# Optimization experiments

Hardware: AMD Instinct MI355X
Metric: run time of the kernel (lower is better)

Reference implementation:

```python
import jax, jax.numpy as jnp
import numpy as np

K_UP = 5
UP = 2
KS = 3
C_IN = 256


def pixel_shuffle(x, r):
    N, C, H, W = x.shape
    x = x.reshape(N, C // (r * r), r, r, H, W)
    return x.transpose(0, 1, 4, 2, 5, 3).reshape(N, C // (r * r), H * r, W * r)


def conv2d(x, w, b, pad):
    y = jax.lax.conv_general_dilated(
        x, w, window_strides=(1, 1), padding=[(pad, pad), (pad, pad)],
        dimension_numbers=('NCHW', 'OIHW', 'NCHW'))
    return y + b[None, :, None, None]


def setup_inputs() -> dict:
    key = jax.random.key(0)
    ks = jax.random.split(key, 7)
    C = C_IN
    Cd = C // 2
    Ce = UP * UP * K_UP * K_UP  # 100
    x = jax.random.normal(ks[0], (4, C, 64, 64), dtype=jnp.float32)
    # kaiming-normal-ish inits, biases small uniform (torch default)
    w_down = jax.random.normal(ks[1], (Cd, C, 1, 1), dtype=jnp.float32) * np.sqrt(2.0 / C)
    b_down = jax.random.uniform(ks[2], (Cd,), dtype=jnp.float32, minval=-0.05, maxval=0.05)
    w_enc = jax.random.normal(ks[3], (Ce, Cd, KS, KS), dtype=jnp.float32) * np.sqrt(2.0 / (Cd * KS * KS))
    b_enc = jax.random.uniform(ks[4], (Ce,), dtype=jnp.float32, minval=-0.05, maxval=0.05)
    w_out = jax.random.normal(ks[5], (C, C, 1, 1), dtype=jnp.float32) * np.sqrt(2.0 / C)
    b_out = jax.random.uniform(ks[6], (C,), dtype=jnp.float32, minval=-0.05, maxval=0.05)
    return {"x": x, "w_down": w_down, "b_down": b_down, "w_enc": w_enc,
            "b_enc": b_enc, "w_out": w_out, "b_out": b_out}


def reference(x, w_down, b_down, w_enc, b_enc, w_out, b_out):
    N, C, H, W = x.shape
    k2 = K_UP * K_UP  # 25
    u2 = UP * UP      # 4
    # kernel prediction branch
    kt = conv2d(x, w_down, b_down, 0)
    kt = conv2d(kt, w_enc, b_enc, KS // 2)
    kt = pixel_shuffle(kt, UP)              # (N, 25, H*UP, W*UP)
    kt = jax.nn.softmax(kt, axis=1)
    # unfold(2,UP,UP).unfold(3,UP,UP) -> (N,25,H,W,UP,UP) -> (N,H,W,25,UP*UP)
    kt = kt.reshape(N, k2, H, UP, W, UP).transpose(0, 2, 4, 1, 3, 5)
    kt = kt.reshape(N, H, W, k2, u2)
    # feature patches: pad then gather k_up x k_up window per pixel
    pad = K_UP // 2
    xp = jnp.pad(x, ((0, 0), (0, 0), (pad, pad), (pad, pad)))
    patches = jnp.stack(
        [xp[:, :, i:i + H, j:j + W] for i in range(K_UP) for j in range(K_UP)],
        axis=-1)                            # (N, C, H, W, 25)
    # per-pixel weighted sum: (N,H,W,C,25) @ (N,H,W,25,u2)
    out = jnp.einsum('nchwk,nhwkp->nchwp', patches, kt)  # (N,C,H,W,u2)
    out = out.transpose(0, 1, 4, 2, 3).reshape(N, C * u2, H, W)
    out = pixel_shuffle(out, UP)            # (N, C, H*UP, W*UP)
    return conv2d(out, w_out, b_out, 0)
```

## Files before the change

### kernel.cpp

```cpp
#include <hip/hip_runtime.h>
#include <hip/hip_bf16.h>


#define NB    4
#define NPIX  4096

typedef short s16x8 __attribute__((ext_vector_type(8)));
typedef float f32x4 __attribute__((ext_vector_type(4)));

#define MFMA16(a, b, c) __builtin_amdgcn_mfma_f32_16x16x32_bf16((a), (b), (c), 0, 0, 0)

__device__ __forceinline__ ushort f2b(float f) {
    __hip_bfloat16 h = __float2bfloat16(f);
    return *(ushort*)&h;
}
__device__ __forceinline__ float b2f(ushort u) {
    unsigned v = ((unsigned)u) << 16;
    return *(float*)&v;
}

__global__ __launch_bounds__(256) void prep_kernel(
    const float* __restrict__ wd, const float* __restrict__ wo,
    const float* __restrict__ we,
    ushort* __restrict__ wdb, ushort* __restrict__ wob, ushort* __restrict__ wrb)
{
    int idx = blockIdx.x * 256 + threadIdx.x;
    if (idx < 32768) {
        wdb[idx] = f2b(wd[idx]);
    } else if (idx < 98304) {
        int i = idx - 32768;
        wob[i] = f2b(wo[i]);
    } else if (idx < 227328) {
        int i = idx - 98304;
        int co = i / 1152, k = i - co * 1152;
        int tap = k >> 7, c = k & 127;
        float v = (co < 100) ? we[(co * 128 + c) * 9 + tap] : 0.0f;
        wrb[i] = f2b(v);
    }
}

__global__ __launch_bounds__(256) void transpose_cast_kernel(
    const float* __restrict__ X, ushort* __restrict__ Xt)
{
    __shared__ ushort xs[64][264];
    const int n = blockIdx.y, p0 = blockIdx.x * 64;
    const int tid = threadIdx.x;
    const float* Xn = X + (size_t)n * 256 * NPIX;

    #pragma unroll
    for (int j = 0; j < 16; j++) {
        float4 v = *(const float4*)&Xn[(size_t)tid * NPIX + p0 + j * 4];
        xs[j * 4 + 0][tid] = f2b(v.x);
        xs[j * 4 + 1][tid] = f2b(v.y);
        xs[j * 4 + 2][tid] = f2b(v.z);
        xs[j * 4 + 3][tid] = f2b(v.w);
    }
    __syncthreads();
    #pragma unroll
    for (int i = 0; i < 8; i++) {
        int flat = tid + 256 * i;
        int pix = flat >> 5, c16 = flat & 31;
        s16x8 v = *(const s16x8*)&xs[pix][c16 * 8];
        *(s16x8*)&Xt[((size_t)(n * NPIX + p0 + pix)) * 256 + c16 * 8] = v;
    }
}

template<int COUT, bool BIAS>
__global__ __launch_bounds__(256, 1) void gemm_mfma_kernel(
    const ushort* __restrict__ Xt,
    const ushort* __restrict__ Wb,
    const float* __restrict__ bias,
    ushort* __restrict__ Out)
{
    __shared__ ushort xs[64][264];
    const int n = blockIdx.y, p0 = blockIdx.x * 64;
    const int tid = threadIdx.x, lane = tid & 63, wid = tid >> 6;
    const int wp = wid >> 1, wc = wid & 1;
    const int l15 = lane & 15, l4 = lane >> 4;
    const ushort* Xn = Xt + (size_t)(n * NPIX + p0) * 256;

    #pragma unroll
    for (int i = 0; i < 8; i++) {
        int flat = tid + 256 * i;
        int row = flat >> 5, ch = flat & 31;
        s16x8 v = *(const s16x8*)&Xn[row * 256 + ch * 8];
        *(s16x8*)&xs[row][ch * 8] = v;
    }
    __syncthreads();

    constexpr int NCF = COUT / 32;
    const int crow = wc * (COUT / 2);

    f32x4 acc[2][NCF] = {};

    #pragma unroll 2
    for (int ks = 0; ks < 8; ks++) {
        int k0 = ks * 32 + l4 * 8;
        s16x8 a0 = *(const s16x8*)&xs[wp * 32 + l15][k0];
        s16x8 a1 = *(const s16x8*)&xs[wp * 32 + 16 + l15][k0];
        #pragma unroll
        for (int cf = 0; cf < NCF; cf++) {
            s16x8 b = *(const s16x8*)&Wb[(size_t)(crow + cf * 16 + l15) * 256 + k0];
            acc[0][cf] = MFMA16(a0, b, acc[0][cf]);
            acc[1][cf] = MFMA16(a1, b, acc[1][cf]);
        }
    }

    #pragma unroll
    for (int pf = 0; pf < 2; pf++) {
        #pragma unroll
        for (int cf = 0; cf < NCF; cf++) {
            int c = crow + cf * 16 + l15;
            float bb = BIAS ? bias[c] : 0.0f;
            #pragma unroll
            for (int r = 0; r < 4; r++) {
                int pix = p0 + wp * 32 + pf * 16 + l4 * 4 + r;
                Out[(size_t)(n * NPIX + pix) * COUT + c] = f2b(acc[pf][cf][r] + bb);
            }
        }
    }
}

__global__ __launch_bounds__(256, 1) void conv_mfma_kernel(
    const ushort* __restrict__ T1t,
    const ushort* __restrict__ Wr,
    const float* __restrict__ Benc,
    float* __restrict__ E)
{
    __shared__ ushort hs[100][136];
    const int n = blockIdx.y, tile = blockIdx.x;
    const int h0 = (tile >> 3) * 8, w0 = (tile & 7) * 8;
    const int tid = threadIdx.x, lane = tid & 63, wid = tid >> 6;
    const int l15 = lane & 15, l4 = lane >> 4;

    for (int u = tid; u < 1600; u += 256) {
        int hp = u >> 4, ch = u & 15;
        int r = hp / 10, s = hp - r * 10;
        int gh = h0 - 1 + r, gw = w0 - 1 + s;
        s16x8 v = {};
        if ((unsigned)gh < 64u && (unsigned)gw < 64u)
            v = *(const s16x8*)&T1t[((size_t)n * NPIX + gh * 64 + gw) * 128 + ch * 8];
        *(s16x8*)&hs[hp][ch * 8] = v;
    }
    __syncthreads();

    const int pl = wid * 16 + l15;
    const int ph = pl >> 3, pw = pl & 7;

    f32x4 acc[7] = {};

    for (int tap = 0; tap < 9; tap++) {
        int dy = tap / 3, dx = tap - dy * 3;
        int hp = (ph + dy) * 10 + (pw + dx);
        const ushort* hrow = &hs[hp][l4 * 8];
        const ushort* wrow = &Wr[(size_t)l15 * 1152 + tap * 128 + l4 * 8];
        #pragma unroll
        for (int cb = 0; cb < 4; cb++) {
            s16x8 b = *(const s16x8*)&hrow[cb * 32];
            #pragma unroll
            for (int mf = 0; mf < 7; mf++) {
                s16x8 a = *(const s16x8*)&wrow[(size_t)mf * 16 * 1152 + cb * 32];
                acc[mf] = MFMA16(a, b, acc[mf]);
            }
        }
    }

    const int gpix = (h0 + ph) * 64 + w0 + pw;
    #pragma unroll
    for (int mf = 0; mf < 7; mf++) {
        #pragma unroll
        for (int r = 0; r < 4; r++) {
            int co = mf * 16 + l4 * 4 + r;
            if (co < 100)
                E[((size_t)n * 100 + co) * NPIX + gpix] = acc[mf][r] + Benc[co];
        }
    }
}

__global__ __launch_bounds__(256) void carafe_kernel(
    const float* __restrict__ E,
    const ushort* __restrict__ XOt,
    const float* __restrict__ Bout,
    float* __restrict__ Z)
{
    __shared__ __attribute__((aligned(16))) float sm[25][64][4];
    __shared__ float xs[64][145];

    const int n = blockIdx.z, oc = blockIdx.y, tile = blockIdx.x;
    const int th0 = (tile >> 3) * 8, tw0 = (tile & 7) * 8;
    const int tid = threadIdx.x;

    {
        int p = tid & 3, pix = tid >> 2;
        int gh = th0 + (pix >> 3), gw = tw0 + (pix & 7);
        const float* En = E + (size_t)n * 100 * NPIX + gh * 64 + gw;
        float v[25];
        float mx = -1e30f;
        #pragma unroll
        for (int k = 0; k < 25; k++) {
            v[k] = En[(size_t)(k * 4 + p) * NPIX];
            mx = fmaxf(mx, v[k]);
        }
        float s = 0.0f;
        #pragma unroll
        for (int k = 0; k < 25; k++) { v[k] = __expf(v[k] - mx); s += v[k]; }
        float inv = 1.0f / s;
        #pragma unroll
        for (int k = 0; k < 25; k++) sm[k][pix][p] = v[k] * inv;
    }

    for (int u = tid; u < 2304; u += 256) {
        int hp = u >> 4, cg = u & 15;
        int r = hp / 12, s = hp - r * 12;
        int gh = th0 - 2 + r, gw = tw0 - 2 + s;
        float v0 = 0.f, v1 = 0.f, v2 = 0.f, v3 = 0.f;
        if ((unsigned)gh < 64u && (unsigned)gw < 64u) {
            const ushort* src = &XOt[((size_t)n * NPIX + gh * 64 + gw) * 256 + oc * 64 + cg * 4];
            ushort4 raw = *(const ushort4*)src;
            v0 = b2f(raw.x); v1 = b2f(raw.y); v2 = b2f(raw.z); v3 = b2f(raw.w);
        }
        xs[cg * 4 + 0][hp] = v0;
        xs[cg * 4 + 1][hp] = v1;
        xs[cg * 4 + 2][hp] = v2;
        xs[cg * 4 + 3][hp] = v3;
    }
    __syncthreads();

    const int pix = tid & 63;
    const int og = tid >> 6;
    const int ph = pix >> 3, pw = pix & 7;

    float acc[16][4] = {};
    for (int k = 0; k < 25; k++) {
        int di = k / 5, dj = k - di * 5;
        float4 wv = *(const float4*)&sm[k][pix][0];
        int base = (ph + di) * 12 + pw + dj;
        #pragma unroll
        for (int i = 0; i < 16; i++) {
            float xv = xs[og * 16 + i][base];
            acc[i][0] += xv * wv.x;
            acc[i][1] += xv * wv.y;
            acc[i][2] += xv * wv.z;
            acc[i][3] += xv * wv.w;
        }
    }

    const int gh = th0 + ph, gw = tw0 + pw;
    #pragma unroll
    for (int i = 0; i < 16; i++) {
        int o = oc * 64 + og * 16 + i;
        float bb = Bout[o];
        float2 r0 = make_float2(acc[i][0] + bb, acc[i][1] + bb);
        float2 r1 = make_float2(acc[i][2] + bb, acc[i][3] + bb);
        size_t base = (((size_t)n * 256 + o) * 128 + 2 * gh) * 128 + 2 * gw;
        *(float2*)&Z[base]       = r0;
        *(float2*)&Z[base + 128] = r1;
    }
}

extern "C" void kernel_launch(void* const* d_in, const int* in_sizes, int n_in,
                              void* d_out, int out_size, void* d_ws, size_t ws_size,
                              hipStream_t stream) {
    const float* x      = (const float*)d_in[0];
    const float* w_down = (const float*)d_in[1];
    const float* b_down = (const float*)d_in[2];
    const float* w_enc  = (const float*)d_in[3];
    const float* b_enc  = (const float*)d_in[4];
    const float* w_out  = (const float*)d_in[5];
    const float* b_out  = (const float*)d_in[6];
    float* z = (float*)d_out;

    ushort* xT  = (ushort*)d_ws;
    ushort* t1T = xT + 4194304;
    ushort* xoT = t1T + 2097152;
    float*  e   = (float*)(xoT + 4194304);
    ushort* wdb = (ushort*)(e + 1638400);
    ushort* wob = wdb + 32768;
    ushort* wrb = wob + 65536;

    prep_kernel<<<888, 256, 0, stream>>>(w_down, w_out, w_enc, wdb, wob, wrb);
    transpose_cast_kernel<<<dim3(64, NB), 256, 0, stream>>>(x, xT);
    gemm_mfma_kernel<128, true><<<dim3(64, NB), 256, 0, stream>>>(xT, wdb, b_down, t1T);
    gemm_mfma_kernel<256, false><<<dim3(64, NB), 256, 0, stream>>>(xT, wob, nullptr, xoT);
    conv_mfma_kernel<<<dim3(64, NB), 256, 0, stream>>>(t1T, wrb, b_enc, e);
    carafe_kernel<<<dim3(64, 4, NB), 256, 0, stream>>>(e, xoT, b_out, z);
}
```

Measured before the change: 175.9 us.

## Fuse transpose with dual GEMM and fuse encoder conv into CARAFE kernel

The transpose/cast kernel and the two 1x1 GEMMs become a single kernel that reads fp32 X directly and computes both the down projection and the output projection against concatenated weights. The 3x3 encoder conv is fused into the CARAFE kernel, which keeps the encoder logits in shared memory instead of a global fp32 buffer and covers all 256 output channels per block. This cuts launches and removes the round trips through global memory for xT and E. In exchange, the CARAFE grid shrinks from 1024 to 256 blocks, each larger and with serialized phases, so less work runs in parallel and the conv stage uses only half the waves.

New measurement: 170.1 us. -3.3%, faster.

```diff
diff --git a/kernel.cpp b/kernel.cpp
--- a/kernel.cpp
+++ b/kernel.cpp
@@ -22,14 +22,12 @@
 __global__ __launch_bounds__(256) void prep_kernel(
     const float* __restrict__ wd, const float* __restrict__ wo,
     const float* __restrict__ we,
-    ushort* __restrict__ wdb, ushort* __restrict__ wob, ushort* __restrict__ wrb)
+    ushort* __restrict__ wcomb, ushort* __restrict__ wrb)
 {
     int idx = blockIdx.x * 256 + threadIdx.x;
-    if (idx < 32768) {
-        wdb[idx] = f2b(wd[idx]);
-    } else if (idx < 98304) {
-        int i = idx - 32768;
-        wob[i] = f2b(wo[i]);
+    if (idx < 98304) {
+        float v = (idx < 32768) ? wd[idx] : wo[idx - 32768];
+        wcomb[idx] = f2b(v);
     } else if (idx < 227328) {
         int i = idx - 98304;
         int co = i / 1152, k = i - co * 1152;
@@ -39,101 +37,95 @@
     }
 }
 
-__global__ __launch_bounds__(256) void transpose_cast_kernel(
-    const float* __restrict__ X, ushort* __restrict__ Xt)
+__global__ __launch_bounds__(512, 1) void dual_gemm_kernel(
+    const float*  __restrict__ X,
+    const ushort* __restrict__ Wcomb,
+    const float*  __restrict__ b_down,
+    ushort* __restrict__ T1t,
+    ushort* __restrict__ XOt)
 {
-    __shared__ ushort xs[64][264];
-    const int n = blockIdx.y, p0 = blockIdx.x * 64;
-    const int tid = threadIdx.x;
-    const float* Xn = X + (size_t)n * 256 * NPIX;
-
-    #pragma unroll
-    for (int j = 0; j < 16; j++) {
-        float4 v = *(const float4*)&Xn[(size_t)tid * NPIX + p0 + j * 4];
-        xs[j * 4 + 0][tid] = f2b(v.x);
-        xs[j * 4 + 1][tid] = f2b(v.y);
-        xs[j * 4 + 2][tid] = f2b(v.z);
-        xs[j * 4 + 3][tid] = f2b(v.w);
-    }
-    __syncthreads();
-    #pragma unroll
-    for (int i = 0; i < 8; i++) {
-        int flat = tid + 256 * i;
-        int pix = flat >> 5, c16 = flat & 31;
-        s16x8 v = *(const s16x8*)&xs[pix][c16 * 8];
-        *(s16x8*)&Xt[((size_t)(n * NPIX + p0 + pix)) * 256 + c16 * 8] = v;
-    }
-}
-
-template<int COUT, bool BIAS>
-__global__ __launch_bounds__(256, 1) void gemm_mfma_kernel(
-    const ushort* __restrict__ Xt,
-    const ushort* __restrict__ Wb,
-    const float* __restrict__ bias,
-    ushort* __restrict__ Out)
-{
-    __shared__ ushort xs[64][264];
+    __shared__ __attribute__((aligned(16))) ushort xs[64][264];
     const int n = blockIdx.y, p0 = blockIdx.x * 64;
     const int tid = threadIdx.x, lane = tid & 63, wid = tid >> 6;
-    const int wp = wid >> 1, wc = wid & 1;
     const int l15 = lane & 15, l4 = lane >> 4;
-    const ushort* Xn = Xt + (size_t)(n * NPIX + p0) * 256;
-
+    const float* Xn = X + (size_t)n * 256 * NPIX + p0;
+
+    {
+        int c = tid >> 1, half = tid & 1;
+        const float* src = Xn + (size_t)c * NPIX + half * 32;
+        #pragma unroll
+        for (int j = 0; j < 8; j++) {
+            float4 v = *(const float4*)&src[j * 4];
+            int pix = half * 32 + j * 4;
+            xs[pix + 0][c] = f2b(v.x);
+            xs[pix + 1][c] = f2b(v.y);
+            xs[pix + 2][c] = f2b(v.z);
+            xs[pix + 3][c] = f2b(v.w);
+        }
+    }
+    __syncthreads();
+
+    const int wp = wid >> 1;
+    const int wc = wid & 1;
+    const int crow = wc * 192;
+
+    f32x4 acc[12] = {};
     #pragma unroll
-    for (int i = 0; i < 8; i++) {
-        int flat = tid + 256 * i;
-        int row = flat >> 5, ch = flat & 31;
-        s16x8 v = *(const s16x8*)&Xn[row * 256 + ch * 8];
-        *(s16x8*)&xs[row][ch * 8] = v;
-    }
-    __syncthreads();
-
-    constexpr int NCF = COUT / 32;
-    const int crow = wc * (COUT / 2);
-
-    f32x4 acc[2][NCF] = {};
-
-    #pragma unroll 2
     for (int ks = 0; ks < 8; ks++) {
         int k0 = ks * 32 + l4 * 8;
-        s16x8 a0 = *(const s16x8*)&xs[wp * 32 + l15][k0];
-        s16x8 a1 = *(const s16x8*)&xs[wp * 32 + 16 + l15][k0];
-        #pragma unroll
-        for (int cf = 0; cf < NCF; cf++) {
-            s16x8 b = *(const s16x8*)&Wb[(size_t)(crow + cf * 16 + l15) * 256 + k0];
-            acc[0][cf] = MFMA16(a0, b, acc[0][cf]);
-            acc[1][cf] = MFMA16(a1, b, acc[1][cf]);
+        s16x8 a = *(const s16x8*)&xs[wp * 16 + l15][k0];
+        #pragma unroll
+        for (int cf = 0; cf < 12; cf++) {
+            s16x8 b = *(const s16x8*)&Wcomb[(size_t)(crow + cf * 16 + l15) * 256 + k0];
+            acc[cf] = MFMA16(a, b, acc[cf]);
         }
     }
 
     #pragma unroll
-    for (int pf = 0; pf < 2; pf++) {
-        #pragma unroll
-        for (int cf = 0; cf < NCF; cf++) {
-            int c = crow + cf * 16 + l15;
-            float bb = BIAS ? bias[c] : 0.0f;
+    for (int cf = 0; cf < 12; cf++) {
+        int cbase = crow + cf * 16;
+        int c = cbase + l15;
+        if (cbase < 128) {
+            float bb = b_down[c];
             #pragma unroll
             for (int r = 0; r < 4; r++) {
-                int pix = p0 + wp * 32 + pf * 16 + l4 * 4 + r;
-                Out[(size_t)(n * NPIX + pix) * COUT + c] = f2b(acc[pf][cf][r] + bb);
-            }
-        }
-    }
-}
-
-__global__ __launch_bounds__(256, 1) void conv_mfma_kernel(
+                int pix = p0 + wp * 16 + l4 * 4 + r;
+                T1t[(size_t)(n * NPIX + pix) * 128 + c] = f2b(acc[cf][r] + bb);
+            }
+        } else {
+            int c2 = c - 128;
+            #pragma unroll
+            for (int r = 0; r < 4; r++) {
+                int pix = p0 + wp * 16 + l4 * 4 + r;
+                XOt[(size_t)(n * NPIX + pix) * 256 + c2] = f2b(acc[cf][r]);
+            }
+        }
+    }
+}
+
+#define SMEM_A 27264
+#define SMEM_TOTAL (SMEM_A + 74240)
+
+__global__ __launch_bounds__(512, 1) void carafe_fused_kernel(
     const ushort* __restrict__ T1t,
     const ushort* __restrict__ Wr,
-    const float* __restrict__ Benc,
-    float* __restrict__ E)
+    const float*  __restrict__ Benc,
+    const ushort* __restrict__ XOt,
+    const float*  __restrict__ Bout,
+    float* __restrict__ Z)
 {
-    __shared__ ushort hs[100][136];
+    __shared__ __attribute__((aligned(16))) char smem[SMEM_TOTAL];
+    ushort (*hs)[136]   = (ushort(*)[136])smem;
+    float  (*sm)[64][4] = (float(*)[64][4])smem;
+    float  (*eld)[101]  = (float(*)[101])(smem + SMEM_A);
+    float  (*xs)[145]   = (float(*)[145])(smem + SMEM_A);
+
     const int n = blockIdx.y, tile = blockIdx.x;
     const int h0 = (tile >> 3) * 8, w0 = (tile & 7) * 8;
     const int tid = threadIdx.x, lane = tid & 63, wid = tid >> 6;
     const int l15 = lane & 15, l4 = lane >> 4;
 
-    for (int u = tid; u < 1600; u += 256) {
+    for (int u = tid; u < 1600; u += 512) {
         int hp = u >> 4, ch = u & 15;
         int r = hp / 10, s = hp - r * 10;
         int gh = h0 - 1 + r, gw = w0 - 1 + s;
@@ -144,117 +136,102 @@
     }
     __syncthreads();
 
-    const int pl = wid * 16 + l15;
-    const int ph = pl >> 3, pw = pl & 7;
-
-    f32x4 acc[7] = {};
-
-    for (int tap = 0; tap < 9; tap++) {
-        int dy = tap / 3, dx = tap - dy * 3;
-        int hp = (ph + dy) * 10 + (pw + dx);
-        const ushort* hrow = &hs[hp][l4 * 8];
-        const ushort* wrow = &Wr[(size_t)l15 * 1152 + tap * 128 + l4 * 8];
-        #pragma unroll
-        for (int cb = 0; cb < 4; cb++) {
-            s16x8 b = *(const s16x8*)&hrow[cb * 32];
-            #pragma unroll
-            for (int mf = 0; mf < 7; mf++) {
-                s16x8 a = *(const s16x8*)&wrow[(size_t)mf * 16 * 1152 + cb * 32];
-                acc[mf] = MFMA16(a, b, acc[mf]);
-            }
-        }
-    }
-
-    const int gpix = (h0 + ph) * 64 + w0 + pw;
-    #pragma unroll
-    for (int mf = 0; mf < 7; mf++) {
-        #pragma unroll
-        for (int r = 0; r < 4; r++) {
-            int co = mf * 16 + l4 * 4 + r;
-            if (co < 100)
-                E[((size_t)n * 100 + co) * NPIX + gpix] = acc[mf][r] + Benc[co];
-        }
-    }
-}
-
-__global__ __launch_bounds__(256) void carafe_kernel(
-    const float* __restrict__ E,
-    const ushort* __restrict__ XOt,
-    const float* __restrict__ Bout,
-    float* __restrict__ Z)
-{
-    __shared__ __attribute__((aligned(16))) float sm[25][64][4];
-    __shared__ float xs[64][145];
-
-    const int n = blockIdx.z, oc = blockIdx.y, tile = blockIdx.x;
-    const int th0 = (tile >> 3) * 8, tw0 = (tile & 7) * 8;
-    const int tid = threadIdx.x;
-
-    {
+    if (wid < 4) {
+        const int pl = wid * 16 + l15;
+        const int ph = pl >> 3, pw = pl & 7;
+        f32x4 acc[7] = {};
+        for (int tap = 0; tap < 9; tap++) {
+            int dy = tap / 3, dx = tap - dy * 3;
+            int hp = (ph + dy) * 10 + pw + dx;
+            const ushort* hrow = &hs[hp][l4 * 8];
+            const ushort* wrow = &Wr[(size_t)l15 * 1152 + tap * 128 + l4 * 8];
+            #pragma unroll
+            for (int cb = 0; cb < 4; cb++) {
+                s16x8 b = *(const s16x8*)&hrow[cb * 32];
+                #pragma unroll
+                for (int mf = 0; mf < 7; mf++) {
+                    s16x8 a = *(const s16x8*)&wrow[(size_t)mf * 16 * 1152 + cb * 32];
+                    acc[mf] = MFMA16(a, b, acc[mf]);
+                }
+            }
+        }
+        #pragma unroll
+        for (int mf = 0; mf < 7; mf++) {
+            #pragma unroll
+            for (int r = 0; r < 4; r++) {
+                int co = mf * 16 + l4 * 4 + r;
+                if (co < 100) eld[pl][co] = acc[mf][r] + Benc[co];
+            }
+        }
+    }
+    __syncthreads();
+
+    if (tid < 256) {
         int p = tid & 3, pix = tid >> 2;
-        int gh = th0 + (pix >> 3), gw = tw0 + (pix & 7);
-        const float* En = E + (size_t)n * 100 * NPIX + gh * 64 + gw;
         float v[25];
         float mx = -1e30f;
         #pragma unroll
+        for (int k = 0; k < 25; k++) { v[k] = eld[pix][4 * k + p]; mx = fmaxf(mx, v[k]); }
+        float ssum = 0.0f;
+        #pragma unroll
+        for (int k = 0; k < 25; k++) { v[k] = __expf(v[k] - mx); ssum += v[k]; }
+        float inv = 1.0f / ssum;
+        #pragma unroll
+        for (int k = 0; k < 25; k++) sm[k][pix][p] = v[k] * inv;
+    }
+    __syncthreads();
+
+    const int pix = tid & 63;
+    const int og8 = tid >> 6;
+    const int ph = pix >> 3, pw = pix & 7;
+    const int cl = og8 >> 2;
+    const int g  = og8 & 3;
+
+    for (int it = 0; it < 2; it++) {
+        for (int u = tid; u < 4608; u += 512) {
+            int hp = u >> 5, cg = u & 31;
+            int r = hp / 12, s = hp - r * 12;
+            int gh = h0 - 2 + r, gw = w0 - 2 + s;
+            float v0 = 0.f, v1 = 0.f, v2 = 0.f, v3 = 0.f;
+            if ((unsigned)gh < 64u && (unsigned)gw < 64u) {
+                ushort4 raw = *(const ushort4*)&XOt[((size_t)n * NPIX + gh * 64 + gw) * 256 + it * 128 + cg * 4];
+                v0 = b2f(raw.x); v1 = b2f(raw.y); v2 = b2f(raw.z); v3 = b2f(raw.w);
+            }
+            xs[cg * 4 + 0][hp] = v0;
+            xs[cg * 4 + 1][hp] = v1;
+            xs[cg * 4 + 2][hp] = v2;
+            xs[cg * 4 + 3][hp] = v3;
+        }
+        __syncthreads();
+
+        float acc[16][4] = {};
         for (int k = 0; k < 25; k++) {
-            v[k] = En[(size_t)(k * 4 + p) * NPIX];
-            mx = fmaxf(mx, v[k]);
-        }
-        float s = 0.0f;
-        #pragma unroll
-        for (int k = 0; k < 25; k++) { v[k] = __expf(v[k] - mx); s += v[k]; }
-        float inv = 1.0f / s;
-        #pragma unroll
-        for (int k = 0; k < 25; k++) sm[k][pix][p] = v[k] * inv;
-    }
-
-    for (int u = tid; u < 2304; u += 256) {
-        int hp = u >> 4, cg = u & 15;
-        int r = hp / 12, s = hp - r * 12;
-        int gh = th0 - 2 + r, gw = tw0 - 2 + s;
-        float v0 = 0.f, v1 = 0.f, v2 = 0.f, v3 = 0.f;
-        if ((unsigned)gh < 64u && (unsigned)gw < 64u) {
-            const ushort* src = &XOt[((size_t)n * NPIX + gh * 64 + gw) * 256 + oc * 64 + cg * 4];
-            ushort4 raw = *(const ushort4*)src;
-            v0 = b2f(raw.x); v1 = b2f(raw.y); v2 = b2f(raw.z); v3 = b2f(raw.w);
-        }
-        xs[cg * 4 + 0][hp] = v0;
-        xs[cg * 4 + 1][hp] = v1;
-        xs[cg * 4 + 2][hp] = v2;
-        xs[cg * 4 + 3][hp] = v3;
-    }
-    __syncthreads();
-
-    const int pix = tid & 63;
-    const int og = tid >> 6;
-    const int ph = pix >> 3, pw = pix & 7;
-
-    float acc[16][4] = {};
-    for (int k = 0; k < 25; k++) {
-        int di = k / 5, dj = k - di * 5;
-        float4 wv = *(const float4*)&sm[k][pix][0];
-        int base = (ph + di) * 12 + pw + dj;
+            int di = k / 5, dj = k - di * 5;
+            float4 wv = *(const float4*)&sm[k][pix][0];
+            int base = (ph + di) * 12 + pw + dj;
+            #pragma unroll
+            for (int i = 0; i < 16; i++) {
+                float xv = xs[cl * 64 + g * 16 + i][base];
+                acc[i][0] += xv * wv.x;
+                acc[i][1] += xv * wv.y;
+                acc[i][2] += xv * wv.z;
+                acc[i][3] += xv * wv.w;
+            }
+        }
+
+        const int gh = h0 + ph, gw = w0 + pw;
+        const int oc = it * 2 + cl;
         #pragma unroll
         for (int i = 0; i < 16; i++) {
-            float xv = xs[og * 16 + i][base];
-            acc[i][0] += xv * wv.x;
-            acc[i][1] += xv * wv.y;
-            acc[i][2] += xv * wv.z;
-            acc[i][3] += xv * wv.w;
-        }
-    }
-
-    const int gh = th0 + ph, gw = tw0 + pw;
-    #pragma unroll
-    for (int i = 0; i < 16; i++) {
-        int o = oc * 64 + og * 16 + i;
-        float bb = Bout[o];
-        float2 r0 = make_float2(acc[i][0] + bb, acc[i][1] + bb);
-        float2 r1 = make_float2(acc[i][2] + bb, acc[i][3] + bb);
-        size_t base = (((size_t)n * 256 + o) * 128 + 2 * gh) * 128 + 2 * gw;
-        *(float2*)&Z[base]       = r0;
-        *(float2*)&Z[base + 128] = r1;
+            int o = oc * 64 + g * 16 + i;
+            float bb = Bout[o];
+            float2 r0 = make_float2(acc[i][0] + bb, acc[i][1] + bb);
+            float2 r1 = make_float2(acc[i][2] + bb, acc[i][3] + bb);
+            size_t zb = (((size_t)n * 256 + o) * 128 + 2 * gh) * 128 + 2 * gw;
+            *(float2*)&Z[zb]       = r0;
+            *(float2*)&Z[zb + 128] = r1;
+        }
+        if (it == 0) __syncthreads();
     }
 }
 
@@ -270,18 +247,12 @@
     const float* b_out  = (const float*)d_in[6];
     float* z = (float*)d_out;
 
-    ushort* xT  = (ushort*)d_ws;
-    ushort* t1T = xT + 4194304;
-    ushort* xoT = t1T + 2097152;
-    float*  e   = (float*)(xoT + 4194304);
-    ushort* wdb = (ushort*)(e + 1638400);
-    ushort* wob = wdb + 32768;
-    ushort* wrb = wob + 65536;
-
-    prep_kernel<<<888, 256, 0, stream>>>(w_down, w_out, w_enc, wdb, wob, wrb);
-    transpose_cast_kernel<<<dim3(64, NB), 256, 0, stream>>>(x, xT);
-    gemm_mfma_kernel<128, true><<<dim3(64, NB), 256, 0, stream>>>(xT, wdb, b_down, t1T);
-    gemm_mfma_kernel<256, false><<<dim3(64, NB), 256, 0, stream>>>(xT, wob, nullptr, xoT);
-    conv_mfma_kernel<<<dim3(64, NB), 256, 0, stream>>>(t1T, wrb, b_enc, e);
-    carafe_kernel<<<dim3(64, 4, NB), 256, 0, stream>>>(e, xoT, b_out, z);
-}
+    ushort* t1T   = (ushort*)d_ws;
+    ushort* xoT   = t1T + 2097152;
+    ushort* wcomb = xoT + 4194304;
+    ushort* wrb   = wcomb + 98304;
+
+    prep_kernel<<<888, 256, 0, stream>>>(w_down, w_out, w_enc, wcomb, wrb);
+    dual_gemm_kernel<<<dim3(64, NB), 512, 0, stream>>>(x, wcomb, b_down, t1T, xoT);
+    carafe_fused_kernel<<<dim3(64, NB), 512, 0, stream>>>(t1T, wrb, b_enc, xoT, b_out, z);
+}
```
